# Optimization experiments

Measured on AMD Instinct MI355X. Metric: run time of the kernel, lower is better.

Reference implementation:

```python
import jax, jax.numpy as jnp
import numpy as np

WIN = 7          # window height/width
P = 10           # prompts_len
HEADS = 12
B0 = 32          # image batch (spa_prompts batch)
NW = 64          # windows per image
NW_TOK = WIN * WIN  # 49


def _relative_position_index(w):
    coords = np.stack(np.meshgrid(np.arange(w), np.arange(w), indexing='ij'))  # [2,w,w]
    flat = coords.reshape(2, -1)                        # [2, w*w]
    rel = flat[:, :, None] - flat[:, None, :]           # [2, w*w, w*w]
    rel = rel.transpose(1, 2, 0).astype(np.int64)       # [w*w, w*w, 2]
    rel[..., 0] += w - 1
    rel[..., 1] += w - 1
    rel[..., 0] *= 2 * w - 1
    return rel.sum(-1)                                  # [w*w, w*w]

REL_IDX = jnp.asarray(_relative_position_index(WIN))    # [49,49] int


def setup_inputs() -> dict:
    key = jax.random.key(0)
    ks = jax.random.split(key, 8)
    dim = 384
    return {
        'x': jax.random.normal(ks[0], (B0 * NW, NW_TOK, dim), jnp.float32),
        'spa_prompts': jax.random.normal(ks[1], (B0, P, dim), jnp.float32),
        'mask': jax.random.normal(ks[2], (NW, NW_TOK, NW_TOK), jnp.float32),
        'bias_table': jax.random.normal(ks[3], (169, HEADS), jnp.float32) * 0.02,
        'w_qkv': jax.random.normal(ks[4], (3 * dim, dim), jnp.float32) * 0.02,
        'b_qkv': jax.random.normal(ks[5], (3 * dim,), jnp.float32) * 0.02,
        'w_proj': jax.random.normal(ks[6], (dim, dim), jnp.float32) * 0.02,
        'b_proj': jax.random.normal(ks[7], (dim,), jnp.float32) * 0.02,
    }


def reference(x, spa_prompts, mask, bias_table, w_qkv, b_qkv, w_proj, b_proj):
    B_, Nw, C = x.shape
    b0 = spa_prompts.shape[0]
    nW = B_ // b0
    hd = C // HEADS
    scale = hd ** -0.5

    # broadcast prompts to every window and prepend
    prompts = jnp.broadcast_to(spa_prompts[:, None], (b0, nW, P, C)).reshape(B_, P, C)
    xc = jnp.concatenate([prompts, x], axis=1)          # [B_, N, C], N = P + Nw
    N = xc.shape[1]

    qkv = xc @ w_qkv.T + b_qkv                          # [B_, N, 3C]
    qkv = qkv.reshape(B_, N, 3, HEADS, hd).transpose(2, 0, 3, 1, 4)
    q, k, v = qkv[0], qkv[1], qkv[2]                    # [B_, H, N, hd]

    attn_weight = jnp.einsum('bhnd,bhmd->bhnm', q, k)   # unscaled, returned

    # relative position bias gathered for the window block, padded over prompt rows/cols
    rpb = bias_table[REL_IDX.reshape(-1)].reshape(NW_TOK, NW_TOK, HEADS)
    rpb = rpb.transpose(2, 0, 1)                        # [H, 49, 49]
    bias_full = jnp.pad(rpb, ((0, 0), (P, 0), (P, 0)))  # [H, N, N]

    attn = attn_weight * scale + bias_full[None]

    mask_full = jnp.pad(mask, ((0, 0), (P, 0), (P, 0)))  # [nW, N, N]
    attn = attn.reshape(b0, nW, HEADS, N, N) + mask_full[None, :, None]
    attn = jax.nn.softmax(attn.reshape(B_, HEADS, N, N), axis=-1)

    out = jnp.einsum('bhnm,bhmd->bnhd', attn, v).reshape(B_, N, C)
    out = out @ w_proj.T + b_proj

    prompts_out = out[:, :P].reshape(b0, nW, P, C).mean(axis=1)
    x_out = out[:, P:]
    return (x_out, attn_weight, prompts_out)
```

## Files before the change

kernel.cpp:

```cpp
#include <hip/hip_runtime.h>
#include <hip/hip_bf16.h>

#define P     10
#define NTOK  59
#define HEADS 12
#define NWTOK 49

#define AW_OFF 38535168
#define PO_OFF 124096512

typedef __attribute__((ext_vector_type(8))) short short8;
typedef __attribute__((ext_vector_type(8))) unsigned short ushort8;
typedef __attribute__((ext_vector_type(4))) float floatx4;
typedef float f4u __attribute__((ext_vector_type(4), aligned(4)));
typedef unsigned int uint_g __attribute__((address_space(1)));
typedef unsigned int uint_l __attribute__((address_space(3)));

__device__ __forceinline__ unsigned short f2b(float f) {
  unsigned u = __builtin_bit_cast(unsigned, f);
  u += 0x7fffu + ((u >> 16) & 1u);
  return (unsigned short)(u >> 16);
}

__device__ __forceinline__ void gll16(const void* g, void* l) {
  __builtin_amdgcn_global_load_lds((const uint_g*)g, (uint_l*)l, 16, 0, 0);
}

__device__ __forceinline__ int xcd_swz(int bid, int nwg) {
  const int q = nwg >> 3, r = nwg & 7;
  const int xcd = bid & 7, ord = bid >> 3;
  return (xcd < r ? xcd * (q + 1) : r * (q + 1) + (xcd - r) * q) + ord;
}

__global__ __launch_bounds__(256) void convert_w_kernel(
    const float* __restrict__ w, unsigned short* __restrict__ wb) {
  const int i = (blockIdx.x * 256 + threadIdx.x) * 8;
  const float4 a = *(const float4*)(w + i);
  const float4 b = *(const float4*)(w + i + 4);
  ushort8 o;
  o[0] = f2b(a.x); o[1] = f2b(a.y); o[2] = f2b(a.z); o[3] = f2b(a.w);
  o[4] = f2b(b.x); o[5] = f2b(b.y); o[6] = f2b(b.z); o[7] = f2b(b.w);
  *(ushort8*)(wb + i) = o;
}

__global__ __launch_bounds__(256) void combo_kernel(
    const float* __restrict__ mask, const float* __restrict__ bias_table,
    float* __restrict__ combo) {
  const int bid = blockIdx.x;
  const int h = bid % HEADS, wnd = bid / HEADS;
#pragma unroll
  for (int e0 = 0; e0 < 4096; e0 += 256) {
    const int e = e0 + threadIdx.x;
    const int ti = e >> 6, tj = e & 63;
    float v = 0.f;
    if (ti >= P && ti < NTOK && tj >= P && tj < NTOK) {
      const int a = ti - P, c = tj - P;
      const int ai = a / 7, aj = a - ai * 7;
      const int bi = c / 7, bj = c - bi * 7;
      const int ridx = (ai - bi + 6) * 13 + (aj - bj + 6);
      v = bias_table[ridx * HEADS + h] + mask[((size_t)wnd * 49 + a) * 49 + c];
    }
    combo[((size_t)bid << 12) + e] = v;
  }
}

__global__ __launch_bounds__(256) void gemm_qkv_kernel(
    const unsigned short* __restrict__ xb, const unsigned short* __restrict__ xp,
    const unsigned short* __restrict__ Bw, const float* __restrict__ b_qkv,
    unsigned short* __restrict__ qkx, unsigned short* __restrict__ qkp) {
  __shared__ unsigned short sbuf[18432];
  unsigned short* Asw = sbuf;
  unsigned short* Bsw = sbuf + 8192;
  const int t = threadIdx.x;
  const int w = t >> 6, lane = t & 63;
  const int lr = lane & 15, lg = lane >> 4;
  const int w0 = w >> 1, w1 = w & 1;
  const int wg = xcd_swz(blockIdx.x, 9 * 787);
  const int cb = wg % 9;
  const int my = wg / 9;
  const bool isP = my >= 784;
  const int n0 = cb * 128;
  const int srow = lane >> 3, cpos = lane & 7;

  floatx4 acc[4][4];
#pragma unroll
  for (int mr = 0; mr < 4; ++mr)
#pragma unroll
    for (int nc = 0; nc < 4; ++nc) acc[mr][nc] = (floatx4)0.f;

  for (int k0 = 0; k0 < 384; k0 += 64) {
#pragma unroll
    for (int i = 0; i < 4; ++i) {
      const int r = (w * 4 + i) * 8 + srow;
      const int c = cpos ^ (r & 7);
      const unsigned short* asrc;
      if (!isP) {
        asrc = xb + (size_t)(my * 128 + r) * 384 + k0 + c * 8;
      } else {
        int mp = (my - 784) * 128 + r;
        if (mp > 319) mp = 319;
        asrc = xp + (size_t)mp * 384 + k0 + c * 8;
      }
      gll16(asrc, Asw + (w * 4 + i) * 512);
      gll16(Bw + (size_t)(n0 + r) * 384 + k0 + c * 8, Bsw + (w * 4 + i) * 512);
    }
    __syncthreads();
#pragma unroll
    for (int kh = 0; kh < 2; ++kh) {
      short8 af[4], bf[4];
#pragma unroll
      for (int mr = 0; mr < 4; ++mr) {
        const int r = w0 * 64 + mr * 16 + lr;
        af[mr] = *(const short8*)(Asw + r * 64 + (((kh * 4 + lg) ^ (r & 7)) * 8));
      }
#pragma unroll
      for (int nc = 0; nc < 4; ++nc) {
        const int r = w1 * 64 + nc * 16 + lr;
        bf[nc] = *(const short8*)(Bsw + r * 64 + (((kh * 4 + lg) ^ (r & 7)) * 8));
      }
#pragma unroll
      for (int mr = 0; mr < 4; ++mr)
#pragma unroll
        for (int nc = 0; nc < 4; ++nc)
          acc[mr][nc] = __builtin_amdgcn_mfma_f32_16x16x32_bf16(
              af[mr], bf[nc], acc[mr][nc], 0, 0, 0);
    }
    __syncthreads();
  }

  const int sec = cb / 3;
  const int nis = (cb - sec * 3) * 128;
  float bias[4];
#pragma unroll
  for (int nc = 0; nc < 4; ++nc)
    bias[nc] = b_qkv[n0 + w1 * 64 + nc * 16 + lr];

  unsigned short* rp = sbuf + w * 4608;
#pragma unroll
  for (int mr = 0; mr < 4; ++mr)
#pragma unroll
    for (int nc = 0; nc < 4; ++nc)
#pragma unroll
      for (int reg = 0; reg < 4; ++reg)
        rp[(mr * 16 + lg * 4 + reg) * 72 + nc * 16 + lr] =
            f2b(acc[mr][nc][reg] + bias[nc]);
  __syncthreads();

  const int rr = lane;
  unsigned short* dst = nullptr;
  if (!isP) {
    const int m = my * 128 + w0 * 64 + rr;
    const int bb = m / 49, tok = m - bb * 49;
    dst = qkx + ((size_t)(bb * 3 + sec) * 49 + tok) * 384 + nis + w1 * 64;
  } else {
    const int mp = (my - 784) * 128 + w0 * 64 + rr;
    if (mp < 320) {
      const int b0 = mp / 10, ptok = mp - b0 * 10;
      dst = qkp + ((size_t)(b0 * 3 + sec) * 10 + ptok) * 384 + nis + w1 * 64;
    }
  }
  if (dst) {
#pragma unroll
    for (int u = 0; u < 8; ++u)
      *(ushort8*)(dst + u * 8) = *(const ushort8*)(rp + rr * 72 + u * 8);
  }
}

__global__ __launch_bounds__(256) void attn_proj_kernel(
    const unsigned short* __restrict__ qkx, const unsigned short* __restrict__ qkp,
    const float* __restrict__ combo, const unsigned short* __restrict__ wproj,
    const float* __restrict__ b_proj, float* __restrict__ aw_out,
    float* __restrict__ x_out, float* __restrict__ pbuf) {
  __shared__ char lds[74752];
  unsigned short* Obuf = (unsigned short*)lds;
  unsigned short* qs   = (unsigned short*)(lds + 50176);
  unsigned short* ks   = (unsigned short*)(lds + 55296);
  unsigned short* vt   = (unsigned short*)(lds + 60416);
  unsigned short* Bst  = (unsigned short*)(lds + 50176);

  const int b = blockIdx.x;
  const int t = threadIdx.x;
  const int w = t >> 6, lane = t & 63, lr = lane & 15, lg = lane >> 4;
  const float scale = 0.17677669529663687f;
  const int q = w * 16 + lr;

  for (int h = 0; h < HEADS; ++h) {
    __syncthreads();
    if (t < 236) {
      const int row = t >> 2, dc = (t & 3) * 8;
      ushort8 q8, k8, v8;
      if (row < P) {
        const unsigned short* pb =
            qkp + ((size_t)((b >> 6) * 3) * 10 + row) * 384 + h * 32 + dc;
        q8 = *(const ushort8*)(pb);
        k8 = *(const ushort8*)(pb + 10 * 384);
        v8 = *(const ushort8*)(pb + 20 * 384);
      } else {
        const unsigned short* xbp =
            qkx + ((size_t)(b * 3) * 49 + (row - P)) * 384 + h * 32 + dc;
        q8 = *(const ushort8*)(xbp);
        k8 = *(const ushort8*)(xbp + 49 * 384);
        v8 = *(const ushort8*)(xbp + 98 * 384);
      }
      *(ushort8*)(qs + row * 40 + dc) = q8;
      *(ushort8*)(ks + row * 40 + dc) = k8;
#pragma unroll
      for (int j = 0; j < 8; ++j) vt[(dc + j) * 74 + row] = v8[j];
    } else {
      const int e = t - 236;
#pragma unroll
      for (int jj = 0; jj < 8; ++jj) {
        const int f = e * 8 + jj;
        vt[(f / 5) * 74 + 59 + (f % 5)] = 0;
      }
    }
    __syncthreads();

    const short8 qa = *(const short8*)(qs + q * 40 + lg * 8);
    floatx4 sacc[4];
#pragma unroll
    for (int nt = 0; nt < 4; ++nt) {
      const short8 kb = *(const short8*)(ks + (nt * 16 + lr) * 40 + lg * 8);
      sacc[nt] =
          __builtin_amdgcn_mfma_f32_16x16x32_bf16(kb, qa, (floatx4)0.f, 0, 0, 0);
    }

    if (q < NTOK) {
      float* rowp = aw_out + ((size_t)(b * HEADS + h)) * 3481 + q * 59;
#pragma unroll
      for (int nt = 0; nt < 3; ++nt)
        *(f4u*)(rowp + nt * 16 + lg * 4) = __builtin_bit_cast(f4u, sacc[nt]);
      if (lg < 2) {
        *(f4u*)(rowp + 48 + lg * 4) = __builtin_bit_cast(f4u, sacc[3]);
      } else if (lg == 2) {
        rowp[56] = sacc[3][0]; rowp[57] = sacc[3][1]; rowp[58] = sacc[3][2];
      }
    }

    const float* comb =
        combo + (((size_t)((b & 63) * HEADS + h)) << 12) + q * 64;
    float ev[4][4];
    float mx = -3.0e38f;
#pragma unroll
    for (int nt = 0; nt < 4; ++nt) {
      const float4 c4 = *(const float4*)(comb + nt * 16 + lg * 4);
      const float cc[4] = {c4.x, c4.y, c4.z, c4.w};
#pragma unroll
      for (int reg = 0; reg < 4; ++reg) {
        const int kk2 = nt * 16 + lg * 4 + reg;
        const float v = (q < NTOK && kk2 < NTOK)
                            ? fmaf(sacc[nt][reg], scale, cc[reg])
                            : -3.0e38f;
        ev[nt][reg] = v;
        mx = fmaxf(mx, v);
      }
    }
    mx = fmaxf(mx, __shfl_xor(mx, 16));
    mx = fmaxf(mx, __shfl_xor(mx, 32));
    float sm = 0.f;
#pragma unroll
    for (int nt = 0; nt < 4; ++nt)
#pragma unroll
      for (int reg = 0; reg < 4; ++reg) {
        const float e = __expf(ev[nt][reg] - mx);
        ev[nt][reg] = e;
        sm += e;
      }
    sm += __shfl_xor(sm, 16);
    sm += __shfl_xor(sm, 32);
    const float inv = 1.0f / sm;

    unsigned pk[4][2];
#pragma unroll
    for (int nt = 0; nt < 4; ++nt)
#pragma unroll
      for (int pp = 0; pp < 2; ++pp)
        pk[nt][pp] = (unsigned)f2b(ev[nt][2 * pp] * inv) |
                     ((unsigned)f2b(ev[nt][2 * pp + 1] * inv) << 16);

    floatx4 oacc[2];
    oacc[0] = (floatx4)0.f; oacc[1] = (floatx4)0.f;
#pragma unroll
    for (int kk = 0; kk < 2; ++kk) {
      unsigned W4[4];
#pragma unroll
      for (int jp = 0; jp < 4; ++jp) {
        const int srcl = lr + 16 * (2 * (lg & 1) + (jp >> 1));
        const int lo = __shfl((int)pk[2 * kk][jp & 1], srcl);
        const int hi = __shfl((int)pk[2 * kk + 1][jp & 1], srcl);
        W4[jp] = (lg >> 1) ? (unsigned)hi : (unsigned)lo;
      }
      uint4 wu; wu.x = W4[0]; wu.y = W4[1]; wu.z = W4[2]; wu.w = W4[3];
      const short8 pa = __builtin_bit_cast(short8, wu);
#pragma unroll
      for (int nt = 0; nt < 2; ++nt) {
        const short8 vb =
            *(const short8*)(vt + (nt * 16 + lr) * 74 + kk * 32 + lg * 8);
        oacc[nt] =
            __builtin_amdgcn_mfma_f32_16x16x32_bf16(pa, vb, oacc[nt], 0, 0, 0);
      }
    }

#pragma unroll
    for (int nt = 0; nt < 2; ++nt)
#pragma unroll
      for (int reg = 0; reg < 4; ++reg)
        Obuf[(w * 16 + lg * 4 + reg) * 392 + h * 32 + nt * 16 + lr] =
            f2b(oacc[nt][reg]);
  }
  __syncthreads();

  floatx4 pacc[12];
#pragma unroll
  for (int nh = 0; nh < 2; ++nh) {
#pragma unroll
    for (int i = 0; i < 12; ++i) pacc[i] = (floatx4)0.f;
    for (int kch = 0; kch < 6; ++kch) {
      __syncthreads();
#pragma unroll
      for (int i = 0; i < 6; ++i) {
        const int g = w * 6 + i;
        const int r = g * 8 + (lane >> 3);
        const int c = (lane & 7) ^ (r & 7);
        gll16(wproj + (size_t)(nh * 192 + r) * 384 + kch * 64 + c * 8,
              Bst + g * 512);
      }
      __syncthreads();
#pragma unroll
      for (int kh = 0; kh < 2; ++kh) {
        const short8 af = *(const short8*)(Obuf + (w * 16 + lr) * 392 +
                                           kch * 64 + kh * 32 + lg * 8);
#pragma unroll
        for (int nc = 0; nc < 12; ++nc) {
          const int nr = nc * 16 + lr;
          const short8 bf =
              *(const short8*)(Bst + nr * 64 + (((kh * 4 + lg) ^ (nr & 7)) * 8));
          pacc[nc] =
              __builtin_amdgcn_mfma_f32_16x16x32_bf16(af, bf, pacc[nc], 0, 0, 0);
        }
      }
    }
#pragma unroll
    for (int nc = 0; nc < 12; ++nc) {
      const int n = nh * 192 + nc * 16 + lr;
      const float bias = b_proj[n];
#pragma unroll
      for (int reg = 0; reg < 4; ++reg) {
        const int row = w * 16 + lg * 4 + reg;
        if (row < NTOK) {
          float* dst = (row >= P)
              ? x_out + ((size_t)(b * NWTOK + row - P)) * 384 + n
              : pbuf + ((size_t)(b * P + row)) * 384 + n;
          *dst = pacc[nc][reg] + bias;
        }
      }
    }
  }
}

__global__ __launch_bounds__(256) void reduce_prompts_kernel(
    const float* __restrict__ pbuf, float* __restrict__ po) {
  const int o = blockIdx.x * 256 + threadIdx.x;
  const int b0 = o / 3840;
  const int rem = o - b0 * 3840;
  const float* base = pbuf + (size_t)b0 * 64 * 3840 + rem;
  float s = 0.f;
#pragma unroll 8
  for (int w = 0; w < 64; ++w) s += base[(size_t)w * 3840];
  po[o] = s * (1.f / 64.f);
}

extern "C" void kernel_launch(void* const* d_in, const int* in_sizes, int n_in,
                              void* d_out, int out_size, void* d_ws, size_t ws_size,
                              hipStream_t stream) {
  const float* x          = (const float*)d_in[0];
  const float* spa        = (const float*)d_in[1];
  const float* mask       = (const float*)d_in[2];
  const float* bias_table = (const float*)d_in[3];
  const float* w_qkv      = (const float*)d_in[4];
  const float* b_qkv      = (const float*)d_in[5];
  const float* w_proj     = (const float*)d_in[6];
  const float* b_proj     = (const float*)d_in[7];
  float* out = (float*)d_out;

  unsigned short* x_bf     = (unsigned short*)d_ws;
  unsigned short* xp_bf    = (unsigned short*)((char*)d_ws + 77070336ULL);
  unsigned short* wqkv_bf  = (unsigned short*)((char*)d_ws + 77316096ULL);
  unsigned short* qkx      = (unsigned short*)((char*)d_ws + 92798976ULL);
  unsigned short* qkp      = (unsigned short*)((char*)d_ws + 324009984ULL);
  unsigned short* wproj_bf = (unsigned short*)((char*)d_ws + 324747264ULL);
  float*          pbuf     = (float*)((char*)d_ws + 325042176ULL);
  float*          combo    = (float*)((char*)d_ws + 356499456ULL);

  convert_w_kernel<<<18816, 256, 0, stream>>>(x, x_bf);
  convert_w_kernel<<<60, 256, 0, stream>>>(spa, xp_bf);
  convert_w_kernel<<<216, 256, 0, stream>>>(w_qkv, wqkv_bf);
  convert_w_kernel<<<72, 256, 0, stream>>>(w_proj, wproj_bf);
  combo_kernel<<<768, 256, 0, stream>>>(mask, bias_table, combo);
  gemm_qkv_kernel<<<9 * 787, 256, 0, stream>>>(x_bf, xp_bf, wqkv_bf, b_qkv,
                                               qkx, qkp);
  attn_proj_kernel<<<2048, 256, 0, stream>>>(qkx, qkp, combo, wproj_bf, b_proj,
                                             out + AW_OFF, out, pbuf);
  reduce_prompts_kernel<<<480, 256, 0, stream>>>(pbuf, out + PO_OFF);
}
```

Measured before the change: 597.3 us.

## Prefetch next head's QKV and next proj weight tile into registers

```diff
diff --git a/kernel.cpp b/kernel.cpp
--- a/kernel.cpp
+++ b/kernel.cpp
@@ -184,36 +184,38 @@
   const float scale = 0.17677669529663687f;
   const int q = w * 16 + lr;
 
+  ushort8 nq, nk, nv;
+  const int srow_ = t >> 2, sdc = (t & 3) * 8;
+  auto load_head = [&](int h) {
+    if (t < 236) {
+      if (srow_ < P) {
+        const unsigned short* pb =
+            qkp + ((size_t)((b >> 6) * 3) * 10 + srow_) * 384 + h * 32 + sdc;
+        nq = *(const ushort8*)(pb);
+        nk = *(const ushort8*)(pb + 10 * 384);
+        nv = *(const ushort8*)(pb + 20 * 384);
+      } else {
+        const unsigned short* xbp =
+            qkx + ((size_t)(b * 3) * 49 + (srow_ - P)) * 384 + h * 32 + sdc;
+        nq = *(const ushort8*)(xbp);
+        nk = *(const ushort8*)(xbp + 49 * 384);
+        nv = *(const ushort8*)(xbp + 98 * 384);
+      }
+    }
+  };
+
+  if (t < 160) vt[(t / 5) * 74 + 59 + (t % 5)] = 0;
+  load_head(0);
+
   for (int h = 0; h < HEADS; ++h) {
     __syncthreads();
     if (t < 236) {
-      const int row = t >> 2, dc = (t & 3) * 8;
-      ushort8 q8, k8, v8;
-      if (row < P) {
-        const unsigned short* pb =
-            qkp + ((size_t)((b >> 6) * 3) * 10 + row) * 384 + h * 32 + dc;
-        q8 = *(const ushort8*)(pb);
-        k8 = *(const ushort8*)(pb + 10 * 384);
-        v8 = *(const ushort8*)(pb + 20 * 384);
-      } else {
-        const unsigned short* xbp =
-            qkx + ((size_t)(b * 3) * 49 + (row - P)) * 384 + h * 32 + dc;
-        q8 = *(const ushort8*)(xbp);
-        k8 = *(const ushort8*)(xbp + 49 * 384);
-        v8 = *(const ushort8*)(xbp + 98 * 384);
-      }
-      *(ushort8*)(qs + row * 40 + dc) = q8;
-      *(ushort8*)(ks + row * 40 + dc) = k8;
-#pragma unroll
-      for (int j = 0; j < 8; ++j) vt[(dc + j) * 74 + row] = v8[j];
-    } else {
-      const int e = t - 236;
-#pragma unroll
-      for (int jj = 0; jj < 8; ++jj) {
-        const int f = e * 8 + jj;
-        vt[(f / 5) * 74 + 59 + (f % 5)] = 0;
-      }
-    }
+      *(ushort8*)(qs + srow_ * 40 + sdc) = nq;
+      *(ushort8*)(ks + srow_ * 40 + sdc) = nk;
+#pragma unroll
+      for (int j = 0; j < 8; ++j) vt[(sdc + j) * 74 + srow_] = nv[j];
+    }
+    if (h + 1 < HEADS) load_head(h + 1);
     __syncthreads();
 
     const short8 qa = *(const short8*)(qs + q * 40 + lg * 8);
@@ -308,7 +310,20 @@
         Obuf[(w * 16 + lg * 4 + reg) * 392 + h * 32 + nt * 16 + lr] =
             f2b(oacc[nt][reg]);
   }
-  __syncthreads();
+
+  ushort8 bst[6];
+  auto load_proj = [&](int s) {
+    const int nh_ = s / 6, kch_ = s % 6;
+#pragma unroll
+    for (int i = 0; i < 6; ++i) {
+      const int g = w * 6 + i;
+      const int r = g * 8 + (lane >> 3);
+      const int c = (lane & 7) ^ (r & 7);
+      bst[i] = *(const ushort8*)(wproj + (size_t)(nh_ * 192 + r) * 384 +
+                                 kch_ * 64 + c * 8);
+    }
+  };
+  load_proj(0);
 
   floatx4 pacc[12];
 #pragma unroll
@@ -316,15 +331,12 @@
 #pragma unroll
     for (int i = 0; i < 12; ++i) pacc[i] = (floatx4)0.f;
     for (int kch = 0; kch < 6; ++kch) {
+      const int s = nh * 6 + kch;
       __syncthreads();
 #pragma unroll
-      for (int i = 0; i < 6; ++i) {
-        const int g = w * 6 + i;
-        const int r = g * 8 + (lane >> 3);
-        const int c = (lane & 7) ^ (r & 7);
-        gll16(wproj + (size_t)(nh * 192 + r) * 384 + kch * 64 + c * 8,
-              Bst + g * 512);
-      }
+      for (int i = 0; i < 6; ++i)
+        *(ushort8*)(Bst + (size_t)(w * 6 + i) * 512 + lane * 8) = bst[i];
+      if (s + 1 < 12) load_proj(s + 1);
       __syncthreads();
 #pragma unroll
       for (int kh = 0; kh < 2; ++kh) {
```

Measured after the change: 586.9 us. Within noise of the previous version (-1.7%).
